# Optimization experiments

Measured on AMD Instinct MI355X. Metric: run time of the kernel, lower is better.

Reference implementation:

```python
import jax, jax.numpy as jnp
import numpy as np

N, E = 50000, 800000
IN, H, D = 64, 4, 16          # in_feats, num_heads, head_size (IN == H*D -> identity skip)
NT, ET = 2, 2                 # num node / edge types


def setup_inputs() -> dict:
    key = jax.random.key(0)
    ks = jax.random.split(key, 13)
    s = 0.05
    return {
        "x": jax.random.normal(ks[0], (N, IN), jnp.float32),
        # TypedLinear weights: one [in,out] matrix per node type (DGL TypedLinear, no bias)
        "Wk": jax.random.normal(ks[1], (NT, IN, H * D), jnp.float32) * s,
        "Wq": jax.random.normal(ks[2], (NT, IN, H * D), jnp.float32) * s,
        "Wv": jax.random.normal(ks[3], (NT, IN, H * D), jnp.float32) * s,
        "Wa": jax.random.normal(ks[4], (NT, H * D, H * D), jnp.float32) * s,
        # per-head, per-edge-type relation matrices (relation_att / relation_msg)
        "Ratt": jax.random.normal(ks[5], (H, ET, D, D), jnp.float32) * s,
        "Rmsg": jax.random.normal(ks[6], (H, ET, D, D), jnp.float32) * s,
        "pri": jnp.ones((H, ET), jnp.float32),   # relation_pri
        "skip": jnp.ones((NT,), jnp.float32),    # skip gate per node type
        "ntype": jax.random.randint(ks[7], (N,), 0, NT),
        "etype": jax.random.randint(ks[8], (E,), 0, ET),
        "src": jax.random.randint(ks[9], (E,), 0, N),
        "dst": jax.random.randint(ks[10], (E,), 0, N),
    }


def _typed_linear(x, W, types):
    # x:[N,I], W:[T,I,O], types:[N] -> y[n] = x[n] @ W[types[n]]
    # T is tiny (2): compute all types densely, then select per node.
    y_all = jnp.einsum('ni,tio->tno', x, W)
    return y_all[types, jnp.arange(x.shape[0])]


def reference(x, Wk, Wq, Wv, Wa, Ratt, Rmsg, pri, skip, ntype, etype, src, dst):
    n = x.shape[0]
    k = _typed_linear(x, Wk, ntype).reshape(n, H, D)
    q = _typed_linear(x, Wq, ntype).reshape(n, H, D)
    v = _typed_linear(x, Wv, ntype).reshape(n, H, D)
    # relation transforms per edge type, computed once at node level (ET is tiny),
    # then gathered per edge: equivalent to per-edge TypedLinear in DGL's message fn.
    katt = jnp.einsum('nhd,htdf->thnf', k, Ratt)   # [ET,H,N,D]
    vmsg = jnp.einsum('nhd,htdf->thnf', v, Rmsg)   # [ET,H,N,D]
    kw = katt[etype, :, src]                       # [E,H,D]
    m = vmsg[etype, :, src]                        # [E,H,D]
    qd = q[dst]                                    # [E,H,D]
    # attention logits: (K W_att) . Q * relation_pri / sqrt(d)
    a = (kw * qd).sum(-1) * pri[:, etype].T / jnp.sqrt(jnp.float32(D))  # [E,H]
    # edge softmax over incoming edges of each destination node (stable)
    amax = jax.ops.segment_max(a, dst, num_segments=n)                  # [N,H]
    ae = jnp.exp(a - amax[dst])
    asum = jax.ops.segment_sum(ae, dst, num_segments=n)
    attn = ae / asum[dst]                                               # [E,H]
    # scatter-aggregate messages
    h = jax.ops.segment_sum(m * attn[:, :, None], dst, num_segments=n)  # [N,H,D]
    # target-specific output projection (dropout is identity in eval)
    h = _typed_linear(h.reshape(n, H * D), Wa, ntype)                   # [N,H*D]
    # sigmoid-gated skip (in_feats == H*D so identity residual)
    alpha = jax.nn.sigmoid(skip)[ntype][:, None]
    return h * alpha + x * (1.0 - alpha)
```

## Files before the change

kernel.cpp:

```cpp
#include <hip/hip_runtime.h>
#include <math.h>
#include <stdint.h>

#define N_NODES 50000
#define N_EDGES 800000
#define NT_TYPES 2
#define ET_TYPES 2
#define M_COLS 320
#define M_PER_T (64 * M_COLS)
#define PROJ_GRID ((N_NODES + 63) / 64)
#define SCAT_GRID ((N_EDGES + 255) / 256)
#define AGG_GRID (N_NODES / 16)
#define NB_SCAN ((N_NODES + 255) / 256)
#define MAXDEG 64
#define LOG2E 1.44269504088896f
#define HSTRIDE 36

typedef __attribute__((ext_vector_type(8))) short short8v;
typedef __attribute__((ext_vector_type(4))) float float4v;

__device__ __forceinline__ unsigned int f32_to_bf16(float f) {
  unsigned int u = __float_as_uint(f);
  return (u + 0x7FFFu + ((u >> 16) & 1u)) >> 16;
}

__device__ __forceinline__ float row16_sum(float p) {
  int r;
  r = __builtin_amdgcn_update_dpp(0, __float_as_int(p), 0x128, 0xf, 0xf, false);
  p += __int_as_float(r);
  r = __builtin_amdgcn_update_dpp(0, __float_as_int(p), 0x124, 0xf, 0xf, false);
  p += __int_as_float(r);
  r = __builtin_amdgcn_update_dpp(0, __float_as_int(p), 0x122, 0xf, 0xf, false);
  p += __int_as_float(r);
  r = __builtin_amdgcn_update_dpp(0, __float_as_int(p), 0x121, 0xf, 0xf, false);
  p += __int_as_float(r);
  return p;
}

__global__ void prep_kernel(
    const float* __restrict__ Wk, const float* __restrict__ Wq,
    const float* __restrict__ Wv, const float* __restrict__ Wa,
    const float* __restrict__ Ratt, const float* __restrict__ Rmsg,
    const float* __restrict__ pri,
    unsigned short* __restrict__ M2b, unsigned short* __restrict__ Wa2b,
    int* __restrict__ deg) {
  const int idx = blockIdx.x * 256 + threadIdx.x;
  if (idx < N_NODES) deg[idx] = 0;
  if (idx < NT_TYPES * 4096) {
    int t = idx >> 12;
    int rem = idx & 4095;
    int col = rem >> 6, k = rem & 63;
    Wa2b[idx] = (unsigned short)f32_to_bf16(Wa[(size_t)t * 4096 + k * 64 + col]);
  }
  if (idx < NT_TYPES * M_PER_T) {
    int t = idx / M_PER_T;
    int rem = idx % M_PER_T;
    int col = rem / 64;
    int k = rem % 64;
    float val;
    if (col < 64) {
      val = Wq[(size_t)t * 4096 + k * 64 + col];
    } else {
      int cc = col - 64;
      int et = cc >> 7;
      int r = cc & 127;
      int c = r >> 1;
      int half = r & 1;
      int h = c >> 4, f = c & 15;
      const float* W = half ? Wv : Wk;
      const float* R = half ? Rmsg : Ratt;
      float s = 0.f;
#pragma unroll
      for (int d = 0; d < 16; ++d)
        s = fmaf(W[(size_t)t * 4096 + k * 64 + h * 16 + d],
                 R[(((size_t)h * ET_TYPES + et) * 16 + d) * 16 + f], s);
      if (half == 0) s *= pri[h * ET_TYPES + et] * 0.25f * LOG2E;
      val = s;
    }
    M2b[idx] = (unsigned short)f32_to_bf16(val);
  }
}

__global__ __launch_bounds__(256) void projscatter_kernel(
    const float* __restrict__ x,
    const unsigned short* __restrict__ M2b,
    const int* __restrict__ ntype,
    unsigned short* __restrict__ qb, unsigned int* __restrict__ kvb,
    const int* __restrict__ src, const int* __restrict__ dst,
    const int* __restrict__ etype, int* __restrict__ deg,
    int* __restrict__ csr) {
  const int bid = blockIdx.x;
  if (bid >= PROJ_GRID) {
    const int e = (bid - PROJ_GRID) * 256 + threadIdx.x;
    if (e < N_EDGES) {
      int d = dst[e];
      int r = atomicAdd(&deg[d], 1);
      csr[(d << 6) + r] = (etype[e] * N_NODES + src[e]) << 6;
    }
    return;
  }
  const int wave = threadIdx.x >> 6;
  const int lane = threadIdx.x & 63;
  const int base = bid * 64 + wave * 16;
  const int l15 = lane & 15;
  const int lq = lane >> 4;

  const int nidA = min(base + l15, N_NODES - 1);
  const float4* xr = reinterpret_cast<const float4*>(x + (size_t)nidA * 64);
  const float4 xa0 = xr[lq * 2 + 0];
  const float4 xa1 = xr[lq * 2 + 1];
  const float4 xb0 = xr[8 + lq * 2 + 0];
  const float4 xb1 = xr[8 + lq * 2 + 1];
  union { short8v v; unsigned int u[4]; } A0u, A1u;
  A0u.u[0] = f32_to_bf16(xa0.x) | (f32_to_bf16(xa0.y) << 16);
  A0u.u[1] = f32_to_bf16(xa0.z) | (f32_to_bf16(xa0.w) << 16);
  A0u.u[2] = f32_to_bf16(xa1.x) | (f32_to_bf16(xa1.y) << 16);
  A0u.u[3] = f32_to_bf16(xa1.z) | (f32_to_bf16(xa1.w) << 16);
  A1u.u[0] = f32_to_bf16(xb0.x) | (f32_to_bf16(xb0.y) << 16);
  A1u.u[1] = f32_to_bf16(xb0.z) | (f32_to_bf16(xb0.w) << 16);
  A1u.u[2] = f32_to_bf16(xb1.x) | (f32_to_bf16(xb1.y) << 16);
  A1u.u[3] = f32_to_bf16(xb1.z) | (f32_to_bf16(xb1.w) << 16);
  const short8v A0 = A0u.v;
  const short8v A1 = A1u.v;

  const int n0 = min(base + lq * 4 + 0, N_NODES - 1);
  const int n1 = min(base + lq * 4 + 1, N_NODES - 1);
  const int n2 = min(base + lq * 4 + 2, N_NODES - 1);
  const int n3 = min(base + lq * 4 + 3, N_NODES - 1);
  const int t0 = ntype[n0], t1 = ntype[n1], t2 = ntype[n2], t3 = ntype[n3];

#pragma unroll
  for (int ct = 0; ct < 20; ++ct) {
    const int colb = ct * 16 + l15;
    const size_t boff = (size_t)colb * 64 + lq * 8;
    const short8v B00 = *reinterpret_cast<const short8v*>(M2b + boff);
    const short8v B01 = *reinterpret_cast<const short8v*>(M2b + boff + 32);
    const short8v B10 = *reinterpret_cast<const short8v*>(M2b + M_PER_T + boff);
    const short8v B11 = *reinterpret_cast<const short8v*>(M2b + M_PER_T + boff + 32);
    float4v C0 = {0.f, 0.f, 0.f, 0.f};
    C0 = __builtin_amdgcn_mfma_f32_16x16x32_bf16(A0, B00, C0, 0, 0, 0);
    C0 = __builtin_amdgcn_mfma_f32_16x16x32_bf16(A1, B01, C0, 0, 0, 0);
    float4v C1 = {0.f, 0.f, 0.f, 0.f};
    C1 = __builtin_amdgcn_mfma_f32_16x16x32_bf16(A0, B10, C1, 0, 0, 0);
    C1 = __builtin_amdgcn_mfma_f32_16x16x32_bf16(A1, B11, C1, 0, 0, 0);

    const float v0 = t0 ? C1[0] : C0[0];
    const float v1 = t1 ? C1[1] : C0[1];
    const float v2 = t2 ? C1[2] : C0[2];
    const float v3 = t3 ? C1[3] : C0[3];

    if (ct < 4) {
      qb[(size_t)n0 * 64 + colb] = (unsigned short)f32_to_bf16(v0);
      qb[(size_t)n1 * 64 + colb] = (unsigned short)f32_to_bf16(v1);
      qb[(size_t)n2 * 64 + colb] = (unsigned short)f32_to_bf16(v2);
      qb[(size_t)n3 * 64 + colb] = (unsigned short)f32_to_bf16(v3);
    } else {
      const float p0 = __shfl_xor(v0, 1, 64);
      const float p1 = __shfl_xor(v1, 1, 64);
      const float p2 = __shfl_xor(v2, 1, 64);
      const float p3 = __shfl_xor(v3, 1, 64);
      if ((lane & 1) == 0) {
        const int cc = colb - 64;
        const int et = cc >> 7;
        const int c = (cc & 127) >> 1;
        const size_t b0 = ((size_t)et * N_NODES) * 64 + c;
        kvb[b0 + (size_t)n0 * 64] = f32_to_bf16(v0) | (f32_to_bf16(p0) << 16);
        kvb[b0 + (size_t)n1 * 64] = f32_to_bf16(v1) | (f32_to_bf16(p1) << 16);
        kvb[b0 + (size_t)n2 * 64] = f32_to_bf16(v2) | (f32_to_bf16(p2) << 16);
        kvb[b0 + (size_t)n3 * 64] = f32_to_bf16(v3) | (f32_to_bf16(p3) << 16);
      }
    }
  }
}

__device__ __forceinline__ void edge_update(unsigned int wrd, float qd,
                                            float& srun, float& acc) {
  float kw = __uint_as_float(wrd << 16);
  float mv = __uint_as_float(wrd & 0xFFFF0000u);
  float w = __builtin_amdgcn_exp2f(row16_sum(kw * qd));
  srun += w;
  acc = fmaf(mv, w, acc);
}

__global__ __launch_bounds__(256) void agg_out_kernel(
    const unsigned short* __restrict__ qb, const unsigned int* __restrict__ kvb,
    const int* __restrict__ deg, const int* __restrict__ csr,
    const unsigned short* __restrict__ Wa2b, const float* __restrict__ x,
    const float* __restrict__ skip, const int* __restrict__ ntype,
    float* __restrict__ out) {
  __shared__ unsigned int hlds[16 * HSTRIDE];
  const int wave = threadIdx.x >> 6;
  const int lane = threadIdx.x & 63;
  const int base = blockIdx.x * 16;

  for (int half = 0; half < 2; ++half) {
    const int lrowA = wave * 4 + half * 2;
    const int nA = __builtin_amdgcn_readfirstlane(base + lrowA);
    const int nB = __builtin_amdgcn_readfirstlane(base + lrowA + 1);
    const float qdA = __uint_as_float((unsigned int)qb[(size_t)nA * 64 + lane] << 16);
    const float qdB = __uint_as_float((unsigned int)qb[(size_t)nB * 64 + lane] << 16);
    const int eA = __builtin_amdgcn_readfirstlane(deg[nA]);
    const int eB = __builtin_amdgcn_readfirstlane(deg[nB]);
    const int* cA = csr + (nA << 6);
    const int* cB = csr + (nB << 6);

    float sA = 0.f, aA = 0.f, sB = 0.f, aB = 0.f;
    const int m = min(eA, eB);
    int j = 0;
    for (; j + 8 <= m; j += 8) {
      int pA0 = __builtin_amdgcn_readfirstlane(cA[j + 0]);
      int pA1 = __builtin_amdgcn_readfirstlane(cA[j + 1]);
      int pA2 = __builtin_amdgcn_readfirstlane(cA[j + 2]);
      int pA3 = __builtin_amdgcn_readfirstlane(cA[j + 3]);
      int pA4 = __builtin_amdgcn_readfirstlane(cA[j + 4]);
      int pA5 = __builtin_amdgcn_readfirstlane(cA[j + 5]);
      int pA6 = __builtin_amdgcn_readfirstlane(cA[j + 6]);
      int pA7 = __builtin_amdgcn_readfirstlane(cA[j + 7]);
      int pB0 = __builtin_amdgcn_readfirstlane(cB[j + 0]);
      int pB1 = __builtin_amdgcn_readfirstlane(cB[j + 1]);
      int pB2 = __builtin_amdgcn_readfirstlane(cB[j + 2]);
      int pB3 = __builtin_amdgcn_readfirstlane(cB[j + 3]);
      int pB4 = __builtin_amdgcn_readfirstlane(cB[j + 4]);
      int pB5 = __builtin_amdgcn_readfirstlane(cB[j + 5]);
      int pB6 = __builtin_amdgcn_readfirstlane(cB[j + 6]);
      int pB7 = __builtin_amdgcn_readfirstlane(cB[j + 7]);
      unsigned int wA0 = kvb[(unsigned)pA0 + lane];
      unsigned int wA1 = kvb[(unsigned)pA1 + lane];
      unsigned int wA2 = kvb[(unsigned)pA2 + lane];
      unsigned int wA3 = kvb[(unsigned)pA3 + lane];
      unsigned int wA4 = kvb[(unsigned)pA4 + lane];
      unsigned int wA5 = kvb[(unsigned)pA5 + lane];
      unsigned int wA6 = kvb[(unsigned)pA6 + lane];
      unsigned int wA7 = kvb[(unsigned)pA7 + lane];
      unsigned int wB0 = kvb[(unsigned)pB0 + lane];
      unsigned int wB1 = kvb[(unsigned)pB1 + lane];
      unsigned int wB2 = kvb[(unsigned)pB2 + lane];
      unsigned int wB3 = kvb[(unsigned)pB3 + lane];
      unsigned int wB4 = kvb[(unsigned)pB4 + lane];
      unsigned int wB5 = kvb[(unsigned)pB5 + lane];
      unsigned int wB6 = kvb[(unsigned)pB6 + lane];
      unsigned int wB7 = kvb[(unsigned)pB7 + lane];
      edge_update(wA0, qdA, sA, aA);
      edge_update(wB0, qdB, sB, aB);
      edge_update(wA1, qdA, sA, aA);
      edge_update(wB1, qdB, sB, aB);
      edge_update(wA2, qdA, sA, aA);
      edge_update(wB2, qdB, sB, aB);
      edge_update(wA3, qdA, sA, aA);
      edge_update(wB3, qdB, sB, aB);
      edge_update(wA4, qdA, sA, aA);
      edge_update(wB4, qdB, sB, aB);
      edge_update(wA5, qdA, sA, aA);
      edge_update(wB5, qdB, sB, aB);
      edge_update(wA6, qdA, sA, aA);
      edge_update(wB6, qdB, sB, aB);
      edge_update(wA7, qdA, sA, aA);
      edge_update(wB7, qdB, sB, aB);
    }
    for (; j + 4 <= m; j += 4) {
      int pA0 = __builtin_amdgcn_readfirstlane(cA[j + 0]);
      int pA1 = __builtin_amdgcn_readfirstlane(cA[j + 1]);
      int pA2 = __builtin_amdgcn_readfirstlane(cA[j + 2]);
      int pA3 = __builtin_amdgcn_readfirstlane(cA[j + 3]);
      int pB0 = __builtin_amdgcn_readfirstlane(cB[j + 0]);
      int pB1 = __builtin_amdgcn_readfirstlane(cB[j + 1]);
      int pB2 = __builtin_amdgcn_readfirstlane(cB[j + 2]);
      int pB3 = __builtin_amdgcn_readfirstlane(cB[j + 3]);
      unsigned int wA0 = kvb[(unsigned)pA0 + lane];
      unsigned int wA1 = kvb[(unsigned)pA1 + lane];
      unsigned int wA2 = kvb[(unsigned)pA2 + lane];
      unsigned int wA3 = kvb[(unsigned)pA3 + lane];
      unsigned int wB0 = kvb[(unsigned)pB0 + lane];
      unsigned int wB1 = kvb[(unsigned)pB1 + lane];
      unsigned int wB2 = kvb[(unsigned)pB2 + lane];
      unsigned int wB3 = kvb[(unsigned)pB3 + lane];
      edge_update(wA0, qdA, sA, aA);
      edge_update(wB0, qdB, sB, aB);
      edge_update(wA1, qdA, sA, aA);
      edge_update(wB1, qdB, sB, aB);
      edge_update(wA2, qdA, sA, aA);
      edge_update(wB2, qdB, sB, aB);
      edge_update(wA3, qdA, sA, aA);
      edge_update(wB3, qdB, sB, aB);
    }
    int jA = j;
    for (; jA + 4 <= eA; jA += 4) {
      int p0 = __builtin_amdgcn_readfirstlane(cA[jA + 0]);
      int p1 = __builtin_amdgcn_readfirstlane(cA[jA + 1]);
      int p2 = __builtin_amdgcn_readfirstlane(cA[jA + 2]);
      int p3 = __builtin_amdgcn_readfirstlane(cA[jA + 3]);
      unsigned int w0 = kvb[(unsigned)p0 + lane];
      unsigned int w1 = kvb[(unsigned)p1 + lane];
      unsigned int w2 = kvb[(unsigned)p2 + lane];
      unsigned int w3 = kvb[(unsigned)p3 + lane];
      edge_update(w0, qdA, sA, aA);
      edge_update(w1, qdA, sA, aA);
      edge_update(w2, qdA, sA, aA);
      edge_update(w3, qdA, sA, aA);
    }
    for (; jA < eA; ++jA) {
      int p = __builtin_amdgcn_readfirstlane(cA[jA]);
      edge_update(kvb[(unsigned)p + lane], qdA, sA, aA);
    }
    int jB = j;
    for (; jB + 4 <= eB; jB += 4) {
      int p0 = __builtin_amdgcn_readfirstlane(cB[jB + 0]);
      int p1 = __builtin_amdgcn_readfirstlane(cB[jB + 1]);
      int p2 = __builtin_amdgcn_readfirstlane(cB[jB + 2]);
      int p3 = __builtin_amdgcn_readfirstlane(cB[jB + 3]);
      unsigned int w0 = kvb[(unsigned)p0 + lane];
      unsigned int w1 = kvb[(unsigned)p1 + lane];
      unsigned int w2 = kvb[(unsigned)p2 + lane];
      unsigned int w3 = kvb[(unsigned)p3 + lane];
      edge_update(w0, qdB, sB, aB);
      edge_update(w1, qdB, sB, aB);
      edge_update(w2, qdB, sB, aB);
      edge_update(w3, qdB, sB, aB);
    }
    for (; jB < eB; ++jB) {
      int p = __builtin_amdgcn_readfirstlane(cB[jB]);
      edge_update(kvb[(unsigned)p + lane], qdB, sB, aB);
    }

    float hvA = (sA > 0.f) ? (aA / sA) : 0.f;
    float hvB = (sB > 0.f) ? (aB / sB) : 0.f;
    float prA = __shfl_xor(hvA, 1, 64);
    float prB = __shfl_xor(hvB, 1, 64);
    if ((lane & 1) == 0) {
      hlds[lrowA * HSTRIDE + (lane >> 1)] =
          f32_to_bf16(hvA) | (f32_to_bf16(prA) << 16);
      hlds[(lrowA + 1) * HSTRIDE + (lane >> 1)] =
          f32_to_bf16(hvB) | (f32_to_bf16(prB) << 16);
    }
  }
  __syncthreads();

  const int l15 = lane & 15;
  const int lq = lane >> 4;
  const short8v A0 = *reinterpret_cast<const short8v*>(&hlds[l15 * HSTRIDE + lq * 4]);
  const short8v A1 = *reinterpret_cast<const short8v*>(&hlds[l15 * HSTRIDE + 16 + lq * 4]);

  const int n0 = base + lq * 4 + 0;
  const int n1 = base + lq * 4 + 1;
  const int n2 = base + lq * 4 + 2;
  const int n3 = base + lq * 4 + 3;
  const int t0 = ntype[n0], t1 = ntype[n1], t2 = ntype[n2], t3 = ntype[n3];

  const float alpha0 = 1.f / (1.f + __expf(-skip[0]));
  const float alpha1 = 1.f / (1.f + __expf(-skip[1]));

  const int colb = wave * 16 + l15;
  const size_t boff = (size_t)colb * 64 + lq * 8;
  const short8v B00 = *reinterpret_cast<const short8v*>(Wa2b + boff);
  const short8v B01 = *reinterpret_cast<const short8v*>(Wa2b + boff + 32);
  const short8v B10 = *reinterpret_cast<const short8v*>(Wa2b + 4096 + boff);
  const short8v B11 = *reinterpret_cast<const short8v*>(Wa2b + 4096 + boff + 32);
  float4v C0 = {0.f, 0.f, 0.f, 0.f};
  C0 = __builtin_amdgcn_mfma_f32_16x16x32_bf16(A0, B00, C0, 0, 0, 0);
  C0 = __builtin_amdgcn_mfma_f32_16x16x32_bf16(A1, B01, C0, 0, 0, 0);
  float4v C1 = {0.f, 0.f, 0.f, 0.f};
  C1 = __builtin_amdgcn_mfma_f32_16x16x32_bf16(A0, B10, C1, 0, 0, 0);
  C1 = __builtin_amdgcn_mfma_f32_16x16x32_bf16(A1, B11, C1, 0, 0, 0);

  const float al0 = t0 ? alpha1 : alpha0;
  const float al1 = t1 ? alpha1 : alpha0;
  const float al2 = t2 ? alpha1 : alpha0;
  const float al3 = t3 ? alpha1 : alpha0;
  const float v0 = t0 ? C1[0] : C0[0];
  const float v1 = t1 ? C1[1] : C0[1];
  const float v2 = t2 ? C1[2] : C0[2];
  const float v3 = t3 ? C1[3] : C0[3];

  const size_t o0 = (size_t)n0 * 64 + colb;
  const size_t o1 = (size_t)n1 * 64 + colb;
  const size_t o2 = (size_t)n2 * 64 + colb;
  const size_t o3 = (size_t)n3 * 64 + colb;
  out[o0] = v0 * al0 + x[o0] * (1.f - al0);
  out[o1] = v1 * al1 + x[o1] * (1.f - al1);
  out[o2] = v2 * al2 + x[o2] * (1.f - al2);
  out[o3] = v3 * al3 + x[o3] * (1.f - al3);
}

extern "C" void kernel_launch(void* const* d_in, const int* in_sizes, int n_in,
                              void* d_out, int out_size, void* d_ws, size_t ws_size,
                              hipStream_t stream) {
  const float* x    = (const float*)d_in[0];
  const float* Wk   = (const float*)d_in[1];
  const float* Wq   = (const float*)d_in[2];
  const float* Wv   = (const float*)d_in[3];
  const float* Wa   = (const float*)d_in[4];
  const float* Ratt = (const float*)d_in[5];
  const float* Rmsg = (const float*)d_in[6];
  const float* pri  = (const float*)d_in[7];
  const float* skip = (const float*)d_in[8];
  const int* ntype  = (const int*)d_in[9];
  const int* etype  = (const int*)d_in[10];
  const int* src    = (const int*)d_in[11];
  const int* dst    = (const int*)d_in[12];
  float* out = (float*)d_out;

  unsigned short* qb = (unsigned short*)d_ws;
  unsigned int* kvb = (unsigned int*)(qb + (size_t)N_NODES * 64);
  int* deg = (int*)(kvb + (size_t)ET_TYPES * N_NODES * 64);
  int* csr = deg + N_NODES;
  unsigned short* M2b = (unsigned short*)
      (((uintptr_t)(csr + (size_t)N_NODES * MAXDEG) + 255) & ~(uintptr_t)255);
  unsigned short* Wa2b = (unsigned short*)
      (((uintptr_t)(M2b + NT_TYPES * M_PER_T) + 255) & ~(uintptr_t)255);

  prep_kernel<<<NB_SCAN, 256, 0, stream>>>(
      Wk, Wq, Wv, Wa, Ratt, Rmsg, pri, M2b, Wa2b, deg);

  projscatter_kernel<<<PROJ_GRID + SCAT_GRID, 256, 0, stream>>>(
      x, M2b, ntype, qb, kvb, src, dst, etype, deg, csr);

  agg_out_kernel<<<AGG_GRID, 256, 0, stream>>>(
      qb, (const unsigned int*)kvb, deg, csr, Wa2b, x, skip, ntype, out);
}
```

Measured before the change: 101.8 us.

## Bucket edges by destination range before CSR scatter to localize atomics

```diff
diff --git a/kernel.cpp b/kernel.cpp
--- a/kernel.cpp
+++ b/kernel.cpp
@@ -9,9 +9,12 @@
 #define M_COLS 320
 #define M_PER_T (64 * M_COLS)
 #define PROJ_GRID ((N_NODES + 63) / 64)
-#define SCAT_GRID ((N_EDGES + 255) / 256)
+#define EDGE_GRID ((N_EDGES + 255) / 256)
 #define AGG_GRID (N_NODES / 16)
 #define NB_SCAN ((N_NODES + 255) / 256)
+#define NPX (N_NODES / 8)
+#define BCAP 131072
+#define SCAT_GRID (8 * (BCAP / 256))
 #define MAXDEG 64
 #define LOG2E 1.44269504088896f
 #define HSTRIDE 36
@@ -43,9 +46,10 @@
     const float* __restrict__ Ratt, const float* __restrict__ Rmsg,
     const float* __restrict__ pri,
     unsigned short* __restrict__ M2b, unsigned short* __restrict__ Wa2b,
-    int* __restrict__ deg) {
+    int* __restrict__ deg, int* __restrict__ bcnt) {
   const int idx = blockIdx.x * 256 + threadIdx.x;
   if (idx < N_NODES) deg[idx] = 0;
+  if (idx < 8) bcnt[idx] = 0;
   if (idx < NT_TYPES * 4096) {
     int t = idx >> 12;
     int rem = idx & 4095;
@@ -81,22 +85,36 @@
   }
 }
 
-__global__ __launch_bounds__(256) void projscatter_kernel(
+__global__ __launch_bounds__(256) void projbucket_kernel(
     const float* __restrict__ x,
     const unsigned short* __restrict__ M2b,
     const int* __restrict__ ntype,
     unsigned short* __restrict__ qb, unsigned int* __restrict__ kvb,
     const int* __restrict__ src, const int* __restrict__ dst,
-    const int* __restrict__ etype, int* __restrict__ deg,
-    int* __restrict__ csr) {
+    const int* __restrict__ etype, int* __restrict__ bcnt,
+    unsigned long long* __restrict__ bucket) {
   const int bid = blockIdx.x;
   if (bid >= PROJ_GRID) {
+    __shared__ int lcnt[8];
+    __shared__ int lbase[8];
     const int e = (bid - PROJ_GRID) * 256 + threadIdx.x;
-    if (e < N_EDGES) {
-      int d = dst[e];
-      int r = atomicAdd(&deg[d], 1);
-      csr[(d << 6) + r] = (etype[e] * N_NODES + src[e]) << 6;
-    }
+    if (threadIdx.x < 8) lcnt[threadIdx.x] = 0;
+    __syncthreads();
+    int d = 0, rec = 0, r = 0, lpos = 0;
+    const bool valid = (e < N_EDGES);
+    if (valid) {
+      d = dst[e];
+      rec = (etype[e] * N_NODES + src[e]) << 6;
+      r = d / NPX;
+      lpos = atomicAdd(&lcnt[r], 1);
+    }
+    __syncthreads();
+    if (threadIdx.x < 8)
+      lbase[threadIdx.x] = atomicAdd(&bcnt[threadIdx.x], lcnt[threadIdx.x]);
+    __syncthreads();
+    if (valid)
+      bucket[(size_t)r * BCAP + lbase[r] + lpos] =
+          ((unsigned long long)(unsigned)rec << 32) | (unsigned)d;
     return;
   }
   const int wave = threadIdx.x >> 6;
@@ -170,6 +188,21 @@
         kvb[b0 + (size_t)n3 * 64] = f32_to_bf16(v3) | (f32_to_bf16(p3) << 16);
       }
     }
+  }
+}
+
+__global__ void scatter_kernel(const unsigned long long* __restrict__ bucket,
+                               const int* __restrict__ bcnt,
+                               int* __restrict__ deg, int* __restrict__ csr) {
+  const int r = blockIdx.x & 7;
+  const int i = (blockIdx.x >> 3) * 256 + threadIdx.x;
+  const int cnt = __builtin_amdgcn_readfirstlane(bcnt[r]);
+  if (i < cnt) {
+    unsigned long long p = bucket[(size_t)r * BCAP + i];
+    int d = (int)(unsigned)p;
+    int rec = (int)(p >> 32);
+    int rank = atomicAdd(&deg[d], 1);
+    csr[(d << 6) + rank] = rec;
   }
 }
 
@@ -401,18 +434,23 @@
 
   unsigned short* qb = (unsigned short*)d_ws;
   unsigned int* kvb = (unsigned int*)(qb + (size_t)N_NODES * 64);
-  int* deg = (int*)(kvb + (size_t)ET_TYPES * N_NODES * 64);
-  int* csr = deg + N_NODES;
+  int* deg  = (int*)(kvb + (size_t)ET_TYPES * N_NODES * 64);
+  int* bcnt = deg + N_NODES;
+  int* csr  = bcnt + 8;
+  unsigned long long* bucket = (unsigned long long*)
+      (((uintptr_t)(csr + (size_t)N_NODES * MAXDEG) + 255) & ~(uintptr_t)255);
   unsigned short* M2b = (unsigned short*)
-      (((uintptr_t)(csr + (size_t)N_NODES * MAXDEG) + 255) & ~(uintptr_t)255);
+      (((uintptr_t)(bucket + (size_t)8 * BCAP) + 255) & ~(uintptr_t)255);
   unsigned short* Wa2b = (unsigned short*)
       (((uintptr_t)(M2b + NT_TYPES * M_PER_T) + 255) & ~(uintptr_t)255);
 
   prep_kernel<<<NB_SCAN, 256, 0, stream>>>(
-      Wk, Wq, Wv, Wa, Ratt, Rmsg, pri, M2b, Wa2b, deg);
-
-  projscatter_kernel<<<PROJ_GRID + SCAT_GRID, 256, 0, stream>>>(
-      x, M2b, ntype, qb, kvb, src, dst, etype, deg, csr);
+      Wk, Wq, Wv, Wa, Ratt, Rmsg, pri, M2b, Wa2b, deg, bcnt);
+
+  projbucket_kernel<<<PROJ_GRID + EDGE_GRID, 256, 0, stream>>>(
+      x, M2b, ntype, qb, kvb, src, dst, etype, bcnt, bucket);
+
+  scatter_kernel<<<SCAT_GRID, 256, 0, stream>>>(bucket, bcnt, deg, csr);
 
   agg_out_kernel<<<AGG_GRID, 256, 0, stream>>>(
       qb, (const unsigned int*)kvb, deg, csr, Wa2b, x, skip, ntype, out);
```

Result: slower. 143.9 us, median of 3 (+41.4%).
